# Optimization experiments

Measured on AMD Instinct MI355X. Metric: run time of the kernel, lower is better.

Reference implementation:

```python
import jax, jax.numpy as jnp
import numpy as np

HIDDEN = 2048
N_HEADS = 16
N_KV = 4
HEAD_DIM = 128
EPS = 1e-6
B = 8
L = 1024
PREFIX = 256
SUFFIX = L - PREFIX
N_COMPACT = PREFIX + B * SUFFIX  # 6400
T_FULL = B * L                   # 8192
ROPE_THETA = 10000.0


def _radix_indices():
    # full position (b, p) -> compact index
    scatter = np.empty(T_FULL, dtype=np.int64)
    for b in range(B):
        scatter[b * L: b * L + PREFIX] = np.arange(PREFIX)
        scatter[b * L + PREFIX: (b + 1) * L] = PREFIX + b * SUFFIX + np.arange(SUFFIX)
    # compact index -> first full occurrence
    fold = np.empty(N_COMPACT, dtype=np.int64)
    fold[:PREFIX] = np.arange(PREFIX)
    for b in range(B):
        fold[PREFIX + b * SUFFIX: PREFIX + (b + 1) * SUFFIX] = b * L + PREFIX + np.arange(SUFFIX)
    return scatter, fold


def setup_inputs() -> dict:
    key = jax.random.key(0)
    ks = jax.random.split(key, 8)
    scatter_np, fold_np = _radix_indices()
    # per-compact-token positions for RoPE
    pos = np.empty(N_COMPACT, dtype=np.float32)
    pos[:PREFIX] = np.arange(PREFIX)
    for b in range(B):
        pos[PREFIX + b * SUFFIX: PREFIX + (b + 1) * SUFFIX] = PREFIX + np.arange(SUFFIX)
    inv_freq = ROPE_THETA ** (-np.arange(HEAD_DIM // 2, dtype=np.float32) / (HEAD_DIM // 2))
    freqs = pos[:, None] * inv_freq[None, :]  # [N_c, 64]
    s = 0.02
    return {
        "hidden_states": jax.random.normal(ks[0], (N_COMPACT, HIDDEN), jnp.float32),
        "cos": jnp.asarray(np.cos(freqs), jnp.float32),
        "sin": jnp.asarray(np.sin(freqs), jnp.float32),
        "cu_seq_lengths": jnp.arange(B + 1, dtype=jnp.int32) * L,
        "max_seq_len": L,
        "fold_gather": jnp.asarray(fold_np),
        "scatter_indices": jnp.asarray(scatter_np),
        "wq": jax.random.normal(ks[1], (HIDDEN, N_HEADS * HEAD_DIM), jnp.float32) * s,
        "wk": jax.random.normal(ks[2], (HIDDEN, N_KV * HEAD_DIM), jnp.float32) * s,
        "wv": jax.random.normal(ks[3], (HIDDEN, N_KV * HEAD_DIM), jnp.float32) * s,
        "wo": jax.random.normal(ks[4], (N_HEADS * HEAD_DIM, HIDDEN), jnp.float32) * s,
        "q_norm_w": jnp.ones((HEAD_DIM,), jnp.float32),
        "k_norm_w": jnp.ones((HEAD_DIM,), jnp.float32),
    }


def _rmsnorm(x, w):
    xf = x.astype(jnp.float32)
    var = jnp.mean(xf * xf, axis=-1, keepdims=True)
    return (w * (xf * jax.lax.rsqrt(var + EPS))).astype(x.dtype)


def _rope(x, cos, sin):
    # x: [N, H, D]; cos/sin: [N, D/2]
    half = cos.shape[-1]
    x1, x2 = x[..., :half], x[..., half:2 * half]
    c, s = cos[:, None, :], sin[:, None, :]
    return jnp.concatenate([x1 * c - x2 * s, x1 * s + x2 * c], axis=-1)


def reference(hidden_states, cos, sin, cu_seq_lengths, max_seq_len,
              fold_gather, scatter_indices, wq, wk, wv, wo, q_norm_w, k_norm_w):
    N = hidden_states.shape[0]
    q = (hidden_states @ wq).reshape(N, N_HEADS, HEAD_DIM)
    k = (hidden_states @ wk).reshape(N, N_KV, HEAD_DIM)
    v = (hidden_states @ wv).reshape(N, N_KV, HEAD_DIM)
    q = _rope(_rmsnorm(q, q_norm_w), cos, sin)
    k = _rope(_rmsnorm(k, k_norm_w), cos, sin)
    # radix scatter: expand compact tokens to full varlen token stream
    qf = q[scatter_indices].reshape(B, L, N_HEADS, HEAD_DIM)
    kf = k[scatter_indices].reshape(B, L, N_KV, HEAD_DIM)
    vf = v[scatter_indices].reshape(B, L, N_KV, HEAD_DIM)
    group = N_HEADS // N_KV
    kf = jnp.repeat(kf, group, axis=2)
    vf = jnp.repeat(vf, group, axis=2)
    scale = HEAD_DIM ** -0.5
    scores = jnp.einsum('bqhd,bkhd->bhqk', qf, kf) * scale
    causal = jnp.tril(jnp.ones((L, L), dtype=bool))
    scores = jnp.where(causal[None, None], scores, jnp.finfo(scores.dtype).min)
    probs = jax.nn.softmax(scores, axis=-1)
    out = jnp.einsum('bhqk,bkhd->bqhd', probs, vf).reshape(T_FULL, N_HEADS * HEAD_DIM)
    # radix fold: gather back to compact tokens
    out_compact = out[fold_gather]
    return out_compact @ wo
```

## Files before the change

kernel.cpp:

```cpp
#include <hip/hip_runtime.h>
#include <hip/hip_bf16.h>

typedef __bf16 bf16;
typedef __bf16 bf16x4 __attribute__((ext_vector_type(4)));
typedef __bf16 bf16x8 __attribute__((ext_vector_type(8)));
typedef float f32x4 __attribute__((ext_vector_type(4)));

#define HID 2048
#define NHEADS 16
#define NKV 4
#define HD 128
#define NC 6400
#define KVW (NKV * HD)

__device__ __forceinline__ void async_cp16(const bf16* src, bf16* dst_lds) {
  __builtin_amdgcn_global_load_lds(
      (const __attribute__((address_space(1))) void*)src,
      (__attribute__((address_space(3))) void*)dst_lds, 16, 0, 0);
}

__device__ __forceinline__ void xcd_swizzle(int& bx, int& by) {
  int nx = gridDim.x;
  int nwg = nx * gridDim.y;
  int id = by * nx + bx;
  int q = nwg >> 3, r = nwg & 7;
  int xcd = id & 7, idx = id >> 3;
  int nid = (xcd < r ? xcd * (q + 1) : r * (q + 1) + (xcd - r) * q) + idx;
  bx = nid % nx;
  by = nid / nx;
}

__global__ __launch_bounds__(256) void k_cvt(const float* __restrict__ in,
                                             bf16* __restrict__ out) {
  size_t i = ((size_t)blockIdx.x * 256 + threadIdx.x) * 8;
  f32x4 a = *(const f32x4*)(in + i);
  f32x4 b = *(const f32x4*)(in + i + 4);
  bf16x8 t;
  for (int j = 0; j < 4; j++) {
    t[j] = (bf16)a[j];
    t[j + 4] = (bf16)b[j];
  }
  *(bf16x8*)(out + i) = t;
}

__global__ __launch_bounds__(256) void k_transpose(const float* __restrict__ in,
                                                   bf16* __restrict__ out,
                                                   int R, int C) {
  __shared__ bf16 tile[32][33];
  int bc = blockIdx.x * 32, br = blockIdx.y * 32;
  int tx = threadIdx.x & 31, ty = threadIdx.x >> 5;
  for (int i = 0; i < 32; i += 8)
    tile[ty + i][tx] = (bf16)in[(size_t)(br + ty + i) * C + bc + tx];
  __syncthreads();
  for (int i = 0; i < 32; i += 8)
    out[(size_t)(bc + ty + i) * R + br + tx] = tile[tx][ty + i];
}

__device__ __forceinline__ void gemm256_core(
    const bf16* __restrict__ A, const bf16* __restrict__ Bt, int m0, int nloc,
    int K, bf16* AsB, bf16* BsB, f32x4 (&acc)[2][4][4]) {
  const int tid = threadIdx.x;
  const int lane = tid & 63, wave = tid >> 6;
  const int l15 = lane & 15, quad = lane >> 4;
  const int wr = wave >> 2, wc = wave & 3;
  const int r0A = wr * 128 + l15;
  const int r0B = wc * 64 + l15;
  const int colOff0 = (quad * 8) ^ ((l15 & 7) << 3);
  const int colOff1 = (32 + quad * 8) ^ ((l15 & 7) << 3);
  const size_t offS0 =
      (size_t)(tid >> 3) * K + ((((tid & 7) ^ ((tid >> 3) & 7)) << 4) >> 1);
  const size_t offS1 = offS0 + (size_t)64 * K;
  const int dstW0 = wave * 512;
  const int dstW1 = 4096 + wave * 512;
  const bf16* Abase = A + (size_t)m0 * K;
  const bf16* Bbase = Bt + (size_t)nloc * K;
  const int KM = K - 1;

#define STAGE(gb, lds, dbuf, h, kc)                             \
  do {                                                          \
    const bf16* _s = (gb) + (size_t)(h) * 128 * K + (kc);       \
    bf16* _d = (lds) + (dbuf) * 16384 + (h) * 8192;             \
    async_cp16(_s + offS0, _d + dstW0);                         \
    async_cp16(_s + offS1, _d + dstW1);                         \
  } while (0)

#define LDA(dbuf, mh)                                           \
  do {                                                          \
    _Pragma("unroll") for (int i = 0; i < 4; i++) {             \
      int r = r0A + (mh) * 64 + i * 16;                         \
      const bf16* p = AsB + (dbuf) * 16384 + r * 64;            \
      a[i][0] = *(const bf16x8*)(p + colOff0);                  \
      a[i][1] = *(const bf16x8*)(p + colOff1);                  \
    }                                                           \
  } while (0)

#define LDB(dbuf, nh, bb)                                       \
  do {                                                          \
    _Pragma("unroll") for (int j = 0; j < 2; j++) {             \
      int r = r0B + (nh) * 32 + j * 16;                         \
      const bf16* p = BsB + (dbuf) * 16384 + r * 64;            \
      bb[j][0] = *(const bf16x8*)(p + colOff0);                 \
      bb[j][1] = *(const bf16x8*)(p + colOff1);                 \
    }                                                           \
  } while (0)

#define MFMAQ(mh, nh, bb)                                                    \
  do {                                                                       \
    __builtin_amdgcn_s_setprio(1);                                           \
    _Pragma("unroll") for (int i = 0; i < 4; i++)                            \
        _Pragma("unroll") for (int j = 0; j < 2; j++) {                      \
      acc[mh][i][(nh) * 2 + j] = __builtin_amdgcn_mfma_f32_16x16x32_bf16(    \
          a[i][0], bb[j][0], acc[mh][i][(nh) * 2 + j], 0, 0, 0);             \
      acc[mh][i][(nh) * 2 + j] = __builtin_amdgcn_mfma_f32_16x16x32_bf16(    \
          a[i][1], bb[j][1], acc[mh][i][(nh) * 2 + j], 0, 0, 0);             \
    }                                                                        \
    __builtin_amdgcn_s_setprio(0);                                           \
  } while (0)

  STAGE(Abase, AsB, 0, 0, 0);
  STAGE(Abase, AsB, 0, 1, 0);
  STAGE(Bbase, BsB, 0, 0, 0);
  STAGE(Bbase, BsB, 0, 1, 0);
  STAGE(Bbase, BsB, 1, 0, 64);
  STAGE(Bbase, BsB, 1, 1, 64);
  STAGE(Abase, AsB, 1, 0, 64);
  asm volatile("s_waitcnt vmcnt(6)" ::: "memory");
  __builtin_amdgcn_s_barrier();

  bf16x8 a[4][2], b0[2][2], b1[2][2];

  const int NIT = K >> 7;
#pragma unroll 1
  for (int it = 0; it < NIT; ++it) {
    const int kb = it << 7;
    LDA(0, 0);
    LDB(0, 0, b0);
    STAGE(Abase, AsB, 1, 1, (kb + 64) & KM);
    asm volatile("s_waitcnt lgkmcnt(8)");
    __builtin_amdgcn_s_barrier();
    asm volatile("s_waitcnt lgkmcnt(0)" ::: "memory");
    MFMAQ(0, 0, b0);
    __builtin_amdgcn_s_barrier();
    LDB(0, 1, b1);
    __builtin_amdgcn_s_barrier();
    asm volatile("s_waitcnt lgkmcnt(0)" ::: "memory");
    MFMAQ(0, 1, b1);
    __builtin_amdgcn_s_barrier();
    LDA(0, 1);
    STAGE(Bbase, BsB, 0, 0, (kb + 128) & KM);
    __builtin_amdgcn_s_barrier();
    asm volatile("s_waitcnt lgkmcnt(0)" ::: "memory");
    MFMAQ(1, 0, b0);
    __builtin_amdgcn_s_barrier();
    STAGE(Bbase, BsB, 0, 1, (kb + 128) & KM);
    __builtin_amdgcn_s_barrier();
    asm volatile("s_waitcnt lgkmcnt(0)" ::: "memory");
    MFMAQ(1, 1, b1);
    asm volatile("s_waitcnt vmcnt(4)" ::: "memory");
    __builtin_amdgcn_s_barrier();
    LDA(1, 0);
    LDB(1, 0, b0);
    STAGE(Abase, AsB, 0, 0, (kb + 128) & KM);
    asm volatile("s_waitcnt lgkmcnt(8)");
    __builtin_amdgcn_s_barrier();
    asm volatile("s_waitcnt lgkmcnt(0)" ::: "memory");
    MFMAQ(0, 0, b0);
    __builtin_amdgcn_s_barrier();
    LDB(1, 1, b1);
    STAGE(Abase, AsB, 0, 1, (kb + 128) & KM);
    __builtin_amdgcn_s_barrier();
    asm volatile("s_waitcnt lgkmcnt(0)" ::: "memory");
    MFMAQ(0, 1, b1);
    __builtin_amdgcn_s_barrier();
    LDA(1, 1);
    STAGE(Bbase, BsB, 1, 0, (kb + 192) & KM);
    __builtin_amdgcn_s_barrier();
    asm volatile("s_waitcnt lgkmcnt(0)" ::: "memory");
    MFMAQ(1, 0, b0);
    __builtin_amdgcn_s_barrier();
    STAGE(Bbase, BsB, 1, 1, (kb + 192) & KM);
    STAGE(Abase, AsB, 1, 0, (kb + 192) & KM);
    __builtin_amdgcn_s_barrier();
    asm volatile("s_waitcnt lgkmcnt(0)" ::: "memory");
    MFMAQ(1, 1, b1);
    asm volatile("s_waitcnt vmcnt(6)" ::: "memory");
    __builtin_amdgcn_s_barrier();
  }
#undef STAGE
#undef LDA
#undef LDB
#undef MFMAQ
}

__global__ __launch_bounds__(512, 2) void k_proj(const bf16* __restrict__ A,
                                                 const bf16* __restrict__ wqT,
                                                 const bf16* __restrict__ wkT,
                                                 const bf16* __restrict__ wvT,
                                                 bf16* __restrict__ qb,
                                                 bf16* __restrict__ kb,
                                                 bf16* __restrict__ vtb) {
  __shared__ __align__(16) bf16 smem[2][2][256][64];
  int bx = blockIdx.x, by = blockIdx.y;
  xcd_swizzle(bx, by);
  int n0 = bx * 256, m0 = by * 256;

  const bf16* bt;
  int nloc, outsel;
  if (n0 < HID) {
    bt = wqT; nloc = n0; outsel = 0;
  } else if (n0 < HID + KVW) {
    bt = wkT; nloc = n0 - HID; outsel = 1;
  } else {
    bt = wvT; nloc = n0 - HID - KVW; outsel = 2;
  }

  const f32x4 fz = {0.0f, 0.0f, 0.0f, 0.0f};
  f32x4 acc[2][4][4];
#pragma unroll
  for (int mh = 0; mh < 2; mh++)
#pragma unroll
    for (int i = 0; i < 4; i++)
#pragma unroll
      for (int j = 0; j < 4; j++) acc[mh][i][j] = fz;

  gemm256_core(A, bt, m0, nloc, HID, &smem[0][0][0][0], &smem[1][0][0][0], acc);

  int tid = threadIdx.x, lane = tid & 63, wave = tid >> 6;
  int l15 = lane & 15, quad = lane >> 4;
  int wr = wave >> 2, wc = wave & 3;

  if (outsel == 2) {
    asm volatile("s_waitcnt vmcnt(0)" ::: "memory");
    __syncthreads();
    bf16* sm = &smem[0][0][0][0];
#pragma unroll
    for (int mh = 0; mh < 2; mh++)
#pragma unroll
      for (int i = 0; i < 4; i++)
#pragma unroll
        for (int nj = 0; nj < 4; nj++) {
          int col = wc * 64 + nj * 16 + l15;
          int row = wr * 128 + mh * 64 + i * 16 + quad * 4;
          int idx = col * 256 + ((row + ((col & 7) << 3)) & 255);
          bf16x4 v4 = {(bf16)acc[mh][i][nj][0], (bf16)acc[mh][i][nj][1],
                       (bf16)acc[mh][i][nj][2], (bf16)acc[mh][i][nj][3]};
          *(bf16x4*)&sm[idx] = v4;
        }
    __syncthreads();
#pragma unroll
    for (int p = 0; p < 4; p++) {
      int cc = p * 64 + (tid >> 3);
      int h = tid & 7;
#pragma unroll
      for (int j = 0; j < 4; j++) {
        int row8 = h * 32 + j * 8;
        bf16x8 v =
            *(const bf16x8*)&sm[cc * 256 + ((row8 + ((cc & 7) << 3)) & 255)];
        *(bf16x8*)(vtb + (size_t)(nloc + cc) * NC + m0 + row8) = v;
      }
    }
  } else {
#pragma unroll
    for (int mh = 0; mh < 2; mh++)
#pragma unroll
      for (int i = 0; i < 4; i++)
#pragma unroll
        for (int nj = 0; nj < 4; nj++)
#pragma unroll
          for (int r = 0; r < 4; r++) {
            int row = m0 + wr * 128 + mh * 64 + i * 16 + quad * 4 + r;
            int col = nloc + wc * 64 + nj * 16 + l15;
            float v = acc[mh][i][nj][r];
            if (outsel == 0)
              qb[(size_t)row * HID + col] = (bf16)v;
            else
              kb[(size_t)row * KVW + col] = (bf16)v;
          }
  }
}

__global__ __launch_bounds__(512, 2) void k_gemm_out(const bf16* __restrict__ A,
                                                     const bf16* __restrict__ Bt,
                                                     float* __restrict__ C,
                                                     int M, int N, int K) {
  __shared__ __align__(16) bf16 smem[2][2][256][64];
  int bx = blockIdx.x, by = blockIdx.y;
  xcd_swizzle(bx, by);
  int n0 = bx * 256, m0 = by * 256;

  const f32x4 fz = {0.0f, 0.0f, 0.0f, 0.0f};
  f32x4 acc[2][4][4];
#pragma unroll
  for (int mh = 0; mh < 2; mh++)
#pragma unroll
    for (int i = 0; i < 4; i++)
#pragma unroll
      for (int j = 0; j < 4; j++) acc[mh][i][j] = fz;

  gemm256_core(A, Bt, m0, n0, K, &smem[0][0][0][0], &smem[1][0][0][0], acc);

  int tid = threadIdx.x, lane = tid & 63, wave = tid >> 6;
  int l15 = lane & 15, quad = lane >> 4;
  int wr = wave >> 2, wc = wave & 3;
#pragma unroll
  for (int mh = 0; mh < 2; mh++)
#pragma unroll
    for (int i = 0; i < 4; i++)
#pragma unroll
      for (int nj = 0; nj < 4; nj++)
#pragma unroll
        for (int r = 0; r < 4; r++) {
          int row = m0 + wr * 128 + mh * 64 + i * 16 + quad * 4 + r;
          int col = n0 + wc * 64 + nj * 16 + l15;
          C[(size_t)row * N + col] = acc[mh][i][nj][r];
        }
}

__global__ __launch_bounds__(256) void k_normrope(bf16* __restrict__ q,
                                                  bf16* __restrict__ k,
                                                  const float* __restrict__ cs,
                                                  const float* __restrict__ sn,
                                                  const float* __restrict__ qw,
                                                  const float* __restrict__ kw) {
  int pair = blockIdx.x * 4 + (threadIdx.x >> 6);
  int lane = threadIdx.x & 63;
  int n = pair / 20, hh = pair % 20;
  bf16* base;
  const float* w;
  if (hh < 16) {
    base = q + (size_t)n * HID + hh * HD;
    w = qw;
  } else {
    base = k + (size_t)n * KVW + (hh - 16) * HD;
    w = kw;
  }
  float x1 = (float)base[lane], x2 = (float)base[lane + 64];
  float ss = x1 * x1 + x2 * x2;
  for (int o = 32; o; o >>= 1) ss += __shfl_xor(ss, o);
  float inv = rsqrtf(ss * (1.0f / 128.0f) + 1e-6f);
  float x1n = x1 * inv * w[lane];
  float x2n = x2 * inv * w[lane + 64];
  float c = cs[(size_t)n * 64 + lane];
  float s = sn[(size_t)n * 64 + lane];
  base[lane] = (bf16)(x1n * c - x2n * s);
  base[lane + 64] = (bf16)(x1n * s + x2n * c);
}

__global__ __launch_bounds__(256, 3) void k_attn(const bf16* __restrict__ qb,
                                                 const bf16* __restrict__ kb,
                                                 const bf16* __restrict__ vt,
                                                 bf16* __restrict__ ob) {
  int t = blockIdx.x;
  int h = blockIdx.y;
  int kh = h >> 2;
  int tid = threadIdx.x;
  int lane = tid & 63, wave = tid >> 6;
  int l15 = lane & 15, quad = lane >> 4;

  int b, p0, nbase;
  if (t < 96) {
    int ti = 11 - (t >> 3);
    b = t & 7;
    p0 = 256 + ti * 64;
    nbase = 256 + b * 768 + ti * 64;
  } else {
    int pt = 99 - t;
    b = 0;
    p0 = pt * 64;
    nbase = pt * 64;
  }

  __shared__ __align__(16) bf16 Ks[64][136];
  __shared__ __align__(16) bf16 Vs[128][72];
  __shared__ __align__(16) bf16 Ps[4][16][72];

  const bf16* kp0 = kb + (size_t)(tid >> 4) * KVW + kh * HD + (tid & 15) * 8;
  const bf16* vp0 = vt + (size_t)(kh * HD + (tid >> 3)) * NC + (tid & 7) * 8;
  bf16* kd0 = &Ks[tid >> 4][(tid & 15) * 8];
  bf16* vd0 = &Vs[tid >> 3][(tid & 7) * 8];

  bf16x8 aq[4];
  {
    const bf16* qp =
        qb + (size_t)(nbase + wave * 16 + l15) * HID + h * HD + quad * 8;
#pragma unroll
    for (int ks = 0; ks < 4; ks++) aq[ks] = *(const bf16x8*)(qp + ks * 32);
  }
  int qpos[4];
#pragma unroll
  for (int r = 0; r < 4; r++) qpos[r] = p0 + wave * 16 + quad * 4 + r;

  const f32x4 fz = {0.0f, 0.0f, 0.0f, 0.0f};
  f32x4 oacc[8];
#pragma unroll
  for (int i = 0; i < 8; i++) oacc[i] = fz;
  float mrow[4], lrow[4];
#pragma unroll
  for (int r = 0; r < 4; r++) {
    mrow[r] = -3.0e38f;
    lrow[r] = 0.0f;
  }
  const float scale = 0.08838834764831845f;

  int nkt = p0 / 64 + 1;

  uint4 kreg[4], vreg[4];
#pragma unroll
  for (int s = 0; s < 4; s++)
    kreg[s] = *(const uint4*)(kp0 + (size_t)s * 16 * KVW);
#pragma unroll
  for (int s = 0; s < 4; s++)
    vreg[s] = *(const uint4*)(vp0 + (size_t)s * 32 * NC);
#pragma unroll
  for (int s = 0; s < 4; s++) *(uint4*)(kd0 + s * 16 * 136) = kreg[s];
#pragma unroll
  for (int s = 0; s < 4; s++) *(uint4*)(vd0 + s * 32 * 72) = vreg[s];
  __syncthreads();

  for (int kt = 0; kt < nkt; kt++) {
    int kpos0 = kt * 64;
    bool hasnext = (kt + 1 < nkt);
    if (hasnext) {
      int kposN = kpos0 + 64;
      int kbaseN = (kposN < 256) ? kposN : 256 + b * 768 + (kposN - 256);
      const bf16* kp = kp0 + (size_t)kbaseN * KVW;
      const bf16* vp = vp0 + kbaseN;
#pragma unroll
      for (int s = 0; s < 4; s++)
        kreg[s] = *(const uint4*)(kp + (size_t)s * 16 * KVW);
#pragma unroll
      for (int s = 0; s < 4; s++)
        vreg[s] = *(const uint4*)(vp + (size_t)s * 32 * NC);
      __builtin_amdgcn_sched_barrier(0);
    }

    bool diag = (kt == nkt - 1);
    float sv[4][4];
#pragma unroll
    for (int nt = 0; nt < 4; nt++) {
      f32x4 z = fz;
      __builtin_amdgcn_s_setprio(1);
#pragma unroll
      for (int ks = 0; ks < 4; ks++) {
        bf16x8 kf = *(const bf16x8*)&Ks[nt * 16 + l15][ks * 32 + quad * 8];
        z = __builtin_amdgcn_mfma_f32_16x16x32_bf16(aq[ks], kf, z, 0, 0, 0);
      }
      __builtin_amdgcn_s_setprio(0);
      int kpos = kpos0 + nt * 16 + l15;
#pragma unroll
      for (int r = 0; r < 4; r++) {
        float v = z[r] * scale;
        if (diag && kpos > qpos[r]) v = -1.0e30f;
        sv[nt][r] = v;
      }
    }
    float alpha[4];
#pragma unroll
    for (int r = 0; r < 4; r++) {
      float mx = fmaxf(fmaxf(sv[0][r], sv[1][r]), fmaxf(sv[2][r], sv[3][r]));
      for (int o = 1; o < 16; o <<= 1) mx = fmaxf(mx, __shfl_xor(mx, o));
      float mnew = fmaxf(mrow[r], mx);
      alpha[r] = __expf(mrow[r] - mnew);
      mrow[r] = mnew;
      float ps = 0.0f;
#pragma unroll
      for (int nt = 0; nt < 4; nt++) {
        float p = __expf(sv[nt][r] - mnew);
        sv[nt][r] = p;
        ps += p;
      }
      for (int o = 1; o < 16; o <<= 1) ps += __shfl_xor(ps, o);
      lrow[r] = lrow[r] * alpha[r] + ps;
    }
#pragma unroll
    for (int i = 0; i < 8; i++)
#pragma unroll
      for (int r = 0; r < 4; r++) oacc[i][r] *= alpha[r];

#pragma unroll
    for (int nt = 0; nt < 4; nt++)
#pragma unroll
      for (int r = 0; r < 4; r++)
        Ps[wave][quad * 4 + r][nt * 16 + l15] = (bf16)sv[nt][r];
    asm volatile("s_waitcnt lgkmcnt(0)" ::: "memory");
    bf16x8 pa[2];
#pragma unroll
    for (int ks = 0; ks < 2; ks++)
      pa[ks] = *(const bf16x8*)&Ps[wave][l15][ks * 32 + quad * 8];
    __builtin_amdgcn_s_setprio(1);
#pragma unroll
    for (int dt = 0; dt < 8; dt++)
#pragma unroll
      for (int ks = 0; ks < 2; ks++) {
        bf16x8 vf = *(const bf16x8*)&Vs[dt * 16 + l15][ks * 32 + quad * 8];
        oacc[dt] =
            __builtin_amdgcn_mfma_f32_16x16x32_bf16(pa[ks], vf, oacc[dt], 0, 0, 0);
      }
    __builtin_amdgcn_s_setprio(0);

    if (hasnext) {
      __syncthreads();
#pragma unroll
      for (int s = 0; s < 4; s++) *(uint4*)(kd0 + s * 16 * 136) = kreg[s];
#pragma unroll
      for (int s = 0; s < 4; s++) *(uint4*)(vd0 + s * 32 * 72) = vreg[s];
      __syncthreads();
    }
  }
#pragma unroll
  for (int r = 0; r < 4; r++) {
    float il = 1.0f / lrow[r];
    bf16* op = ob + (size_t)(nbase + wave * 16 + quad * 4 + r) * HID + h * HD;
#pragma unroll
    for (int dt = 0; dt < 8; dt++) op[dt * 16 + l15] = (bf16)(oacc[dt][r] * il);
  }
}

extern "C" void kernel_launch(void* const* d_in, const int* in_sizes, int n_in,
                              void* d_out, int out_size, void* d_ws,
                              size_t ws_size, hipStream_t stream) {
  const float* hs = (const float*)d_in[0];
  const float* cs = (const float*)d_in[1];
  const float* sn = (const float*)d_in[2];
  const float* wq = (const float*)d_in[7];
  const float* wk = (const float*)d_in[8];
  const float* wv = (const float*)d_in[9];
  const float* wo = (const float*)d_in[10];
  const float* qnw = (const float*)d_in[11];
  const float* knw = (const float*)d_in[12];
  float* out = (float*)d_out;

  bf16* hsb = (bf16*)d_out;
  bf16* wqT = hsb + (size_t)NC * HID;
  bf16* wkT = wqT + (size_t)HID * HID;
  bf16* wvT = wkT + (size_t)KVW * HID;
  bf16* qb  = (bf16*)d_in[0];
  bf16* ab  = qb + (size_t)NC * HID;
  bf16* woT = qb;
  bf16* kb  = (bf16*)d_ws;
  bf16* vtb = kb + (size_t)NC * KVW;

  k_cvt<<<dim3(NC * HID / (256 * 8)), 256, 0, stream>>>(hs, hsb);
  k_transpose<<<dim3(HID / 32, HID / 32), 256, 0, stream>>>(wq, wqT, HID, HID);
  k_transpose<<<dim3(KVW / 32, HID / 32), 256, 0, stream>>>(wk, wkT, HID, KVW);
  k_transpose<<<dim3(KVW / 32, HID / 32), 256, 0, stream>>>(wv, wvT, HID, KVW);

  k_proj<<<dim3((HID + 2 * KVW) / 256, NC / 256), 512, 0, stream>>>(
      hsb, wqT, wkT, wvT, qb, kb, vtb);

  k_normrope<<<dim3(NC * 20 / 4), 256, 0, stream>>>(qb, kb, cs, sn, qnw, knw);

  k_attn<<<dim3(100, NHEADS), 256, 0, stream>>>(qb, kb, vtb, ab);

  k_transpose<<<dim3(HID / 32, HID / 32), 256, 0, stream>>>(wo, woT, HID, HID);

  k_gemm_out<<<dim3(HID / 256, NC / 256), 512, 0, stream>>>(ab, woT, out, NC, HID, HID);
}
```

Before: 539.8 us.

## Double-buffer attention K/V tiles with async global-to-LDS copies and XOR swizzle

Replaces the register-staged K/V prefetch in the attention kernel with direct global_load_lds async copies into a double-buffered LDS tile. Unpadded tiles use an XOR swizzle to avoid bank conflicts. This removes the register round-trip and one barrier per tile, and frees registers. In exchange it doubles the K/V shared memory and drops the occupancy hint from launch bounds, which may reduce resident blocks per CU.

```diff
diff --git a/kernel.cpp b/kernel.cpp
--- a/kernel.cpp
+++ b/kernel.cpp
@@ -346,10 +346,10 @@
   base[lane + 64] = (bf16)(x1n * s + x2n * c);
 }
 
-__global__ __launch_bounds__(256, 3) void k_attn(const bf16* __restrict__ qb,
-                                                 const bf16* __restrict__ kb,
-                                                 const bf16* __restrict__ vt,
-                                                 bf16* __restrict__ ob) {
+__global__ __launch_bounds__(256) void k_attn(const bf16* __restrict__ qb,
+                                              const bf16* __restrict__ kb,
+                                              const bf16* __restrict__ vt,
+                                              bf16* __restrict__ ob) {
   int t = blockIdx.x;
   int h = blockIdx.y;
   int kh = h >> 2;
@@ -370,14 +370,25 @@
     nbase = pt * 64;
   }
 
-  __shared__ __align__(16) bf16 Ks[64][136];
-  __shared__ __align__(16) bf16 Vs[128][72];
+  __shared__ __align__(16) bf16 Ks[2][64][128];
+  __shared__ __align__(16) bf16 Vs[2][128][64];
   __shared__ __align__(16) bf16 Ps[4][16][72];
 
-  const bf16* kp0 = kb + (size_t)(tid >> 4) * KVW + kh * HD + (tid & 15) * 8;
-  const bf16* vp0 = vt + (size_t)(kh * HD + (tid >> 3)) * NC + (tid & 7) * 8;
-  bf16* kd0 = &Ks[tid >> 4][(tid & 15) * 8];
-  bf16* vd0 = &Vs[tid >> 3][(tid & 7) * 8];
+#define STAGE_KV(buf, kbase)                                                  \
+  do {                                                                        \
+    _Pragma("unroll") for (int i = 0; i < 4; i++) {                           \
+      int rowK = wave * 16 + i * 4 + quad;                                    \
+      async_cp16(kb + (size_t)((kbase) + rowK) * KVW + kh * HD +              \
+                     ((l15 ^ ((i * 4 + quad) & 7)) << 3),                     \
+                 &Ks[buf][0][0] + (wave * 4 + i) * 512);                      \
+    }                                                                         \
+    _Pragma("unroll") for (int i = 0; i < 4; i++) {                           \
+      int dV = wave * 32 + i * 8 + (lane >> 3);                               \
+      async_cp16(vt + (size_t)(kh * HD + dV) * NC + (kbase) +                 \
+                     (((lane & 7) ^ (lane >> 3)) << 3),                       \
+                 &Vs[buf][0][0] + (wave * 4 + i) * 512);                      \
+    }                                                                         \
+  } while (0)
 
   bf16x8 aq[4];
   {
@@ -401,36 +412,22 @@
     lrow[r] = 0.0f;
   }
   const float scale = 0.08838834764831845f;
+  const int swzc = (l15 & 7) << 3;
 
   int nkt = p0 / 64 + 1;
 
-  uint4 kreg[4], vreg[4];
-#pragma unroll
-  for (int s = 0; s < 4; s++)
-    kreg[s] = *(const uint4*)(kp0 + (size_t)s * 16 * KVW);
-#pragma unroll
-  for (int s = 0; s < 4; s++)
-    vreg[s] = *(const uint4*)(vp0 + (size_t)s * 32 * NC);
-#pragma unroll
-  for (int s = 0; s < 4; s++) *(uint4*)(kd0 + s * 16 * 136) = kreg[s];
-#pragma unroll
-  for (int s = 0; s < 4; s++) *(uint4*)(vd0 + s * 32 * 72) = vreg[s];
+  STAGE_KV(0, 0);
+  asm volatile("s_waitcnt vmcnt(0)" ::: "memory");
   __syncthreads();
 
+  int cur = 0;
   for (int kt = 0; kt < nkt; kt++) {
     int kpos0 = kt * 64;
     bool hasnext = (kt + 1 < nkt);
     if (hasnext) {
       int kposN = kpos0 + 64;
       int kbaseN = (kposN < 256) ? kposN : 256 + b * 768 + (kposN - 256);
-      const bf16* kp = kp0 + (size_t)kbaseN * KVW;
-      const bf16* vp = vp0 + kbaseN;
-#pragma unroll
-      for (int s = 0; s < 4; s++)
-        kreg[s] = *(const uint4*)(kp + (size_t)s * 16 * KVW);
-#pragma unroll
-      for (int s = 0; s < 4; s++)
-        vreg[s] = *(const uint4*)(vp + (size_t)s * 32 * NC);
+      STAGE_KV(cur ^ 1, kbaseN);
       __builtin_amdgcn_sched_barrier(0);
     }
 
@@ -442,7 +439,8 @@
       __builtin_amdgcn_s_setprio(1);
 #pragma unroll
       for (int ks = 0; ks < 4; ks++) {
-        bf16x8 kf = *(const bf16x8*)&Ks[nt * 16 + l15][ks * 32 + quad * 8];
+        bf16x8 kf =
+            *(const bf16x8*)&Ks[cur][nt * 16 + l15][(ks * 32 + quad * 8) ^ swzc];
         z = __builtin_amdgcn_mfma_f32_16x16x32_bf16(aq[ks], kf, z, 0, 0, 0);
       }
       __builtin_amdgcn_s_setprio(0);
@@ -492,21 +490,20 @@
     for (int dt = 0; dt < 8; dt++)
 #pragma unroll
       for (int ks = 0; ks < 2; ks++) {
-        bf16x8 vf = *(const bf16x8*)&Vs[dt * 16 + l15][ks * 32 + quad * 8];
+        bf16x8 vf =
+            *(const bf16x8*)&Vs[cur][dt * 16 + l15][(ks * 32 + quad * 8) ^ swzc];
         oacc[dt] =
             __builtin_amdgcn_mfma_f32_16x16x32_bf16(pa[ks], vf, oacc[dt], 0, 0, 0);
       }
     __builtin_amdgcn_s_setprio(0);
 
     if (hasnext) {
+      asm volatile("s_waitcnt vmcnt(0)" ::: "memory");
       __syncthreads();
-#pragma unroll
-      for (int s = 0; s < 4; s++) *(uint4*)(kd0 + s * 16 * 136) = kreg[s];
-#pragma unroll
-      for (int s = 0; s < 4; s++) *(uint4*)(vd0 + s * 32 * 72) = vreg[s];
-      __syncthreads();
+      cur ^= 1;
     }
   }
+#undef STAGE_KV
 #pragma unroll
   for (int r = 0; r < 4; r++) {
     float il = 1.0f / lrow[r];
```

Measured after the change: 451.9 us. 16.3% less time.
